# Kernel tuning notes

Measured on AMD Instinct MI355X. Metric: run time of the kernel, lower is better.

Reference implementation:

```python
import jax, jax.numpy as jnp
import numpy as np

B, S, F_ATT, R, A = 1024, 96, 2048, 512, 512  # batch, att_size, att_feat_size, rnn_size, att_hid_size

def setup_inputs() -> dict:
    key = jax.random.key(0)
    ks = jax.random.split(key, 16)
    def lin(k, out_d, in_d):
        s = 1.0 / np.sqrt(in_d)
        kw, kb = jax.random.split(k)
        return (jax.random.uniform(kw, (out_d, in_d), jnp.float32, -s, s),
                jax.random.uniform(kb, (out_d,), jnp.float32, -s, s))
    W_ae, b_ae = lin(ks[0], R, F_ATT)   # att_embed Linear
    W_c,  b_c  = lin(ks[1], A, R)       # ctx2att
    W_s,  b_s  = lin(ks[2], A, R)       # sentinel_embed
    W_h,  b_h  = lin(ks[3], A, R)       # ho_embed
    W_al, b_al = lin(ks[4], 1, A)       # alpha_net
    W_o,  b_o  = lin(ks[5], R, R)       # att2h
    return {
        'h': jax.random.normal(ks[6], (B, R), jnp.float32),
        'sentinel': jax.random.normal(ks[7], (B, R), jnp.float32),
        'att_feats': jax.random.normal(ks[8], (B, S, F_ATT), jnp.float32),
        'W_ae': W_ae, 'b_ae': b_ae, 'W_c': W_c, 'b_c': b_c,
        'W_s': W_s, 'b_s': b_s, 'W_h': W_h, 'b_h': b_h,
        'W_al': W_al, 'b_al': b_al, 'W_o': W_o, 'b_o': b_o,
    }

def reference(h, sentinel, att_feats, W_ae, b_ae, W_c, b_c, W_s, b_s,
              W_h, b_h, W_al, b_al, W_o, b_o):
    # att_embed: Linear(2048->512) + ReLU (dropout = identity in eval)
    att = jax.nn.relu(jnp.einsum('bsf,rf->bsr', att_feats, W_ae) + b_ae)  # [B,S,R]
    att_embd = jnp.einsum('bsr,ar->bsa', att, W_c) + b_c                   # [B,S,A]
    sent_e = sentinel @ W_s.T + b_s                                        # [B,A]
    h_e = h @ W_h.T + b_h                                                  # [B,A]
    # concat sentinel slot in front of attention features
    img_all = jnp.concatenate([sentinel[:, None, :], att], axis=1)         # [B,S+1,R]
    img_all_embed = jnp.concatenate([sent_e[:, None, :], att_embd], axis=1)  # [B,S+1,A]
    hA = jnp.tanh(img_all_embed + h_e[:, None, :])                         # [B,S+1,A]
    logits = jnp.einsum('bsa,a->bs', hA, W_al[0]) + b_al[0]                # [B,S+1]
    alpha = jax.nn.softmax(logits, axis=-1)
    cHat = jnp.einsum('bs,bsr->br', alpha, img_all)                        # [B,R]
    atten_out = cHat + h
    return jnp.tanh(atten_out @ W_o.T + b_o)                               # [B,R]
```

## Files before the change

### kernel.cpp

```cpp
#include <hip/hip_runtime.h>

#define M1 98304
#define RDIM 512
#define FDIM 2048
#define SDIM 96
#define BM 96
#define BK 64

typedef __attribute__((ext_vector_type(8))) __bf16 bf16x8;
typedef __attribute__((ext_vector_type(4))) float f32x4;

__device__ __forceinline__ float bf2f(unsigned short u){
  union { unsigned int i; float f; } v; v.i = ((unsigned int)u) << 16; return v.f;
}
__device__ __forceinline__ unsigned short f2bf(float f){
  union { float f; unsigned int i; } v; v.f = f;
  unsigned int r = v.i + 0x7FFFu + ((v.i >> 16) & 1u);
  return (unsigned short)(r >> 16);
}
__device__ __forceinline__ unsigned short f2bfn(float f){
  __bf16 b = (__bf16)f;
  return __builtin_bit_cast(unsigned short, b);
}
__device__ __forceinline__ float fast_tanh(float x){
  float e = __expf(2.f * x);
  return 1.f - 2.f / (e + 1.f);
}
__device__ __forceinline__ void gld_lds16(const void* g, void* l){
  __builtin_amdgcn_global_load_lds((const __attribute__((address_space(1))) void*)g,
                                   (__attribute__((address_space(3))) void*)l, 16, 0, 0);
}
__device__ __forceinline__ f32x4 mfma16(bf16x8 a, bf16x8 b, f32x4 c){
  return __builtin_amdgcn_mfma_f32_16x16x32_bf16(a, b, c, 0, 0, 0);
}

__device__ __forceinline__ void cat_store_a(const float* __restrict__ src,
                                            unsigned short* __restrict__ dst, int idx){
  float x = src[idx];
  int r = idx >> 9, c = idx & 511;
  unsigned short hi = f2bf(x);
  unsigned short lo = f2bf(x - bf2f(hi));
  unsigned short* p = dst + (long)r * 1536 + c;
  p[0] = hi; p[512] = lo; p[1024] = hi;
}
__device__ __forceinline__ void cat_store_w(const float* __restrict__ src,
                                            unsigned short* __restrict__ dst, int idx){
  float x = src[idx];
  int r = idx >> 9, c = idx & 511;
  unsigned short hi = f2bf(x);
  unsigned short lo = f2bf(x - bf2f(hi));
  unsigned short* p = dst + (long)r * 1536 + c;
  p[0] = hi; p[512] = hi; p[1024] = lo;
}

__global__ void k_convert(const float* W_ae, const float* W_c, const float* W_s,
                          const float* W_h, const float* W_o,
                          const float* h, const float* sent,
                          unsigned short* W_ae_bf, unsigned short* W_c_bf,
                          unsigned short* W_s_cat, unsigned short* W_h_cat,
                          unsigned short* W_o_cat, unsigned short* h_cat,
                          unsigned short* s_cat){
  int idx = blockIdx.x * 256 + threadIdx.x;
  switch (blockIdx.y) {
    case 0: if (idx < 512*2048) W_ae_bf[idx] = f2bf(W_ae[idx]); break;
    case 1: if (idx < 512*512)  W_c_bf[idx]  = f2bf(W_c[idx]);  break;
    case 2: if (idx < 512*512)  cat_store_w(W_s, W_s_cat, idx); break;
    case 3: if (idx < 512*512)  cat_store_w(W_h, W_h_cat, idx); break;
    case 4: if (idx < 512*512)  cat_store_w(W_o, W_o_cat, idx); break;
    case 5: if (idx < 1024*512) cat_store_a(h, h_cat, idx); break;
    case 6: if (idx < 1024*512) cat_store_a(sent, s_cat, idx); break;
  }
}

__global__ __launch_bounds__(512) void k_fused(
    const float* __restrict__ Af, const unsigned short* __restrict__ Wae,
    const float* __restrict__ b_ae,
    const unsigned short* __restrict__ Wcg, const float* __restrict__ b_c,
    const float* __restrict__ h_e, const float* __restrict__ W_al,
    const float* __restrict__ sent_e, const float* __restrict__ sent,
    const float* __restrict__ hvec, unsigned short* __restrict__ atten_cat){
  __shared__ __align__(16) char smem[155648];
  unsigned short* As   = (unsigned short*)smem;
  unsigned short* Bs   = (unsigned short*)(smem + 24576);
  unsigned short* attL = (unsigned short*)smem;
  unsigned short* Wcs  = (unsigned short*)(smem + 98304);
  float* part = (float*)(smem + 131072);
  float* lg   = (float*)(smem + 131072 + 1536);
  float* alp  = (float*)(smem + 131072 + 1536 + 512);
  float* ssum = (float*)(smem + 131072 + 1536 + 1024);

  const int tid = threadIdx.x;
  const int w = tid >> 6, l = tid & 63;
  const int wm = w >> 2, wn = w & 3;
  const int b = blockIdx.x;
  const long m0 = (long)b * BM;
  const int g = l >> 4, r15 = l & 15;
  const int rs = r15 & 7;

  f32x4 acc[3][8];
#pragma unroll
  for (int i = 0; i < 3; ++i)
#pragma unroll
    for (int j = 0; j < 8; ++j) acc[i][j] = f32x4{0.f,0.f,0.f,0.f};

  {
    const int brow_in = l >> 3;
    const int bswz = (l & 7) ^ brow_in;
    const unsigned short* bbase = Wae + (long)(w*64 + brow_in) * FDIM + bswz*8;
    const int NT = FDIM / BK;

    {
#pragma unroll
      for (int q = 0; q < 8; ++q)
        gld_lds16(bbase + (long)q*8*FDIM, Bs + (w*8+q)*512);
      float4 v[3];
#pragma unroll
      for (int s = 0; s < 3; ++s) {
        int c = tid + s*512, row = c >> 4, kq = c & 15;
        v[s] = *reinterpret_cast<const float4*>(Af + (m0+row)*FDIM + kq*4);
      }
#pragma unroll
      for (int s = 0; s < 3; ++s) {
        int c = tid + s*512, row = c >> 4, kq = c & 15;
        ushort4 pk; pk.x=f2bfn(v[s].x); pk.y=f2bfn(v[s].y); pk.z=f2bfn(v[s].z); pk.w=f2bfn(v[s].w);
        *reinterpret_cast<ushort4*>(&As[row*BK + ((kq ^ ((row&7)<<1))<<2)]) = pk;
      }
    }
    __syncthreads();

    int cb = 0;
    for (int kt = 0; kt < NT; ++kt) {
      const int nb = cb ^ 1;
      float4 v[3];
      const bool more = (kt + 1 < NT);
      if (more) {
        const int kof = (kt+1) * BK;
#pragma unroll
        for (int q = 0; q < 8; ++q)
          gld_lds16(bbase + (long)q*8*FDIM + kof, Bs + nb*32768 + (w*8+q)*512);
#pragma unroll
        for (int s = 0; s < 3; ++s) {
          int c = tid + s*512, row = c >> 4, kq = c & 15;
          v[s] = *reinterpret_cast<const float4*>(Af + (m0+row)*FDIM + kof + kq*4);
        }
      }
#pragma unroll
      for (int hh = 0; hh < 2; ++hh) {
        const int ko = ((g + 4*hh) ^ rs) << 3;
        bf16x8 afr[3], bfr[8];
#pragma unroll
        for (int i = 0; i < 3; ++i)
          afr[i] = *reinterpret_cast<const bf16x8*>(&As[cb*6144 + (wm*48 + i*16 + r15)*BK + ko]);
#pragma unroll
        for (int j = 0; j < 8; ++j)
          bfr[j] = *reinterpret_cast<const bf16x8*>(&Bs[cb*32768 + (wn*128 + j*16 + r15)*BK + ko]);
        __builtin_amdgcn_s_setprio(1);
#pragma unroll
        for (int i = 0; i < 3; ++i)
#pragma unroll
          for (int j = 0; j < 8; ++j)
            acc[i][j] = mfma16(afr[i], bfr[j], acc[i][j]);
        __builtin_amdgcn_s_setprio(0);
      }
      if (more) {
#pragma unroll
        for (int s = 0; s < 3; ++s) {
          int c = tid + s*512, row = c >> 4, kq = c & 15;
          ushort4 pk; pk.x=f2bfn(v[s].x); pk.y=f2bfn(v[s].y); pk.z=f2bfn(v[s].z); pk.w=f2bfn(v[s].w);
          *reinterpret_cast<ushort4*>(&As[nb*6144 + row*BK + ((kq ^ ((row&7)<<1))<<2)]) = pk;
        }
        __syncthreads();
        cb = nb;
      }
    }
  }
  __syncthreads();
  {
    float bb[8];
#pragma unroll
    for (int j = 0; j < 8; ++j) bb[j] = b_ae[wn*128 + j*16 + r15];
#pragma unroll
    for (int i = 0; i < 3; ++i)
#pragma unroll
      for (int r = 0; r < 4; ++r) {
        int row = wm*48 + i*16 + g*4 + r;
        int rs8 = row & 7;
#pragma unroll
        for (int j = 0; j < 8; ++j) {
          int col = wn*128 + j*16 + r15;
          float x = acc[i][j][r] + bb[j];
          x = x > 0.f ? x : 0.f;
          attL[row*512 + (((col>>3) ^ rs8)<<3) + (col&7)] = f2bfn(x);
        }
      }
  }
  __syncthreads();

#pragma unroll
  for (int i = 0; i < 3; ++i)
#pragma unroll
    for (int j = 0; j < 8; ++j) acc[i][j] = f32x4{0.f,0.f,0.f,0.f};
  {
    const int crow = l >> 2;
    const int bsl2 = (l & 3) ^ ((l >> 3) & 3);
    const int rs2 = (r15 >> 1) & 3;
    for (int kt = 0; kt < 16; ++kt) {
#pragma unroll
      for (int i = 0; i < 4; ++i)
        gld_lds16(Wcg + (long)(w*64 + i*16 + crow)*RDIM + kt*32 + bsl2*8,
                  Wcs + w*2048 + i*512);
      __syncthreads();
      bf16x8 afr[3], bfr[8];
#pragma unroll
      for (int i = 0; i < 3; ++i) {
        int ra = wm*48 + i*16 + r15;
        int grp = (kt<<2) + g;
        afr[i] = *reinterpret_cast<const bf16x8*>(&attL[ra*512 + ((grp ^ rs)<<3)]);
      }
#pragma unroll
      for (int j = 0; j < 8; ++j)
        bfr[j] = *reinterpret_cast<const bf16x8*>(&Wcs[(wn*128 + j*16 + r15)*32 + ((g ^ rs2)<<3)]);
      __builtin_amdgcn_s_setprio(1);
#pragma unroll
      for (int i = 0; i < 3; ++i)
#pragma unroll
        for (int j = 0; j < 8; ++j)
          acc[i][j] = mfma16(afr[i], bfr[j], acc[i][j]);
      __builtin_amdgcn_s_setprio(0);
      __syncthreads();
    }
  }
  {
    const float* hrow = h_e + (long)b * RDIM;
    float bb2[8], wa[8], he[8];
#pragma unroll
    for (int j = 0; j < 8; ++j) {
      int n = wn*128 + j*16 + r15;
      bb2[j] = b_c[n]; wa[j] = W_al[n]; he[j] = hrow[n];
    }
#pragma unroll
    for (int i = 0; i < 3; ++i)
#pragma unroll
      for (int r = 0; r < 4; ++r) {
        int lrow = wm*48 + i*16 + g*4 + r;
        float s = 0.f;
#pragma unroll
        for (int j = 0; j < 8; ++j) {
          float x = acc[i][j][r] + bb2[j] + he[j];
          s += fast_tanh(x) * wa[j];
        }
        s += __shfl_xor(s, 1); s += __shfl_xor(s, 2);
        s += __shfl_xor(s, 4); s += __shfl_xor(s, 8);
        if (r15 == 0) part[lrow*4 + wn] = s;
      }
  }
  __syncthreads();
  if (tid < 96)
    lg[1+tid] = part[tid*4+0] + part[tid*4+1] + part[tid*4+2] + part[tid*4+3];
  if (tid < 64) {
    float s = 0.f;
    for (int a = tid; a < 512; a += 64)
      s += fast_tanh(sent_e[(long)b*512 + a] + h_e[(long)b*512 + a]) * W_al[a];
    s += __shfl_xor(s, 1); s += __shfl_xor(s, 2); s += __shfl_xor(s, 4);
    s += __shfl_xor(s, 8); s += __shfl_xor(s, 16); s += __shfl_xor(s, 32);
    if (tid == 0) lg[0] = s;
  }
  __syncthreads();
  if (tid < 64) {
    float m = -1e30f;
    for (int i = tid; i < 97; i += 64) m = fmaxf(m, lg[i]);
#pragma unroll
    for (int k = 1; k < 64; k <<= 1) m = fmaxf(m, __shfl_xor(m, k));
    float ss = 0.f;
    for (int i = tid; i < 97; i += 64) { float e = __expf(lg[i] - m); alp[i] = e; ss += e; }
#pragma unroll
    for (int k = 1; k < 64; k <<= 1) ss += __shfl_xor(ss, k);
    if (tid == 0) ssum[0] = ss;
  }
  __syncthreads();
  if (tid < 97) alp[tid] *= (1.f / ssum[0]);
  __syncthreads();
  {
    const int col = tid;
    const int cg = col >> 3, ch = col & 7;
    float accv = alp[0] * sent[(long)b*512 + col];
#pragma unroll 4
    for (int s = 0; s < SDIM; ++s)
      accv += alp[s+1] * bf2f(attL[s*512 + ((cg ^ (s&7))<<3) + ch]);
    float x = accv + hvec[(long)b*512 + col];
    unsigned short hi = f2bf(x);
    unsigned short lo = f2bf(x - bf2f(hi));
    unsigned short* pp = atten_cat + (long)b*1536 + col;
    pp[0] = hi; pp[512] = lo; pp[1024] = hi;
  }
}

__device__ __forceinline__ void small_gemm_body(
    const unsigned short* __restrict__ Abf, const unsigned short* __restrict__ Wb,
    const float* __restrict__ bias, float* __restrict__ Cout, int do_tanh, int bx,
    unsigned short* As, unsigned short* Bs){
  const int tid = threadIdx.x;
  const int w = tid >> 6, l = tid & 63;
  const int wm = w >> 1, wn = w & 1;
  const int m0 = (bx >> 3) * 64, n0 = (bx & 7) * 64;
  const int K = 1536;
  f32x4 acc[2][2];
#pragma unroll
  for (int i = 0; i < 2; ++i)
#pragma unroll
    for (int j = 0; j < 2; ++j) acc[i][j] = f32x4{0.f,0.f,0.f,0.f};

  const int crow = l >> 2;
  const int bsl = (l & 3) ^ ((l >> 3) & 3);

  for (int kt = 0; kt < 48; ++kt) {
    const int k0 = kt * 32;
    gld_lds16(Abf + (long)(m0 + w*16 + crow)*K + k0 + bsl*8, As + w*512);
    gld_lds16(Wb  + (long)(n0 + w*16 + crow)*K + k0 + bsl*8, Bs + w*512);
    __syncthreads();
    bf16x8 afr[2], bfr[2];
    const int g = l >> 4, r15 = l & 15;
    const int rs2 = (r15 >> 1) & 3;
#pragma unroll
    for (int i = 0; i < 2; ++i)
      afr[i] = *reinterpret_cast<const bf16x8*>(As + (wm*32 + i*16 + r15)*32 + ((g ^ rs2)*8));
#pragma unroll
    for (int j = 0; j < 2; ++j)
      bfr[j] = *reinterpret_cast<const bf16x8*>(Bs + (wn*32 + j*16 + r15)*32 + ((g ^ rs2)*8));
#pragma unroll
    for (int i = 0; i < 2; ++i)
#pragma unroll
      for (int j = 0; j < 2; ++j)
        acc[i][j] = mfma16(afr[i], bfr[j], acc[i][j]);
    __syncthreads();
  }
  const int r15 = l & 15, g = l >> 4;
#pragma unroll
  for (int i = 0; i < 2; ++i)
#pragma unroll
    for (int r = 0; r < 4; ++r) {
      int m = m0 + wm*32 + i*16 + g*4 + r;
#pragma unroll
      for (int j = 0; j < 2; ++j) {
        int n = n0 + wn*32 + j*16 + r15;
        float x = acc[i][j][r] + bias[n];
        if (do_tanh) x = fast_tanh(x);
        Cout[(long)m * 512 + n] = x;
      }
    }
}

__global__ __launch_bounds__(256) void k_gemm_small(
    const unsigned short* __restrict__ Abf, const unsigned short* __restrict__ Wb,
    const float* __restrict__ bias, float* __restrict__ Cout, int do_tanh){
  __shared__ __align__(16) unsigned short As[64*32];
  __shared__ __align__(16) unsigned short Bs[64*32];
  small_gemm_body(Abf, Wb, bias, Cout, do_tanh, blockIdx.x, As, Bs);
}

__global__ __launch_bounds__(256) void k_embed2(
    const unsigned short* __restrict__ h_cat, const unsigned short* __restrict__ W_h_cat,
    const float* __restrict__ b_h, float* __restrict__ h_e,
    const unsigned short* __restrict__ s_cat, const unsigned short* __restrict__ W_s_cat,
    const float* __restrict__ b_s, float* __restrict__ sent_e){
  __shared__ __align__(16) unsigned short As[64*32];
  __shared__ __align__(16) unsigned short Bs[64*32];
  if (blockIdx.y == 0) small_gemm_body(h_cat, W_h_cat, b_h, h_e, 0, blockIdx.x, As, Bs);
  else                 small_gemm_body(s_cat, W_s_cat, b_s, sent_e, 0, blockIdx.x, As, Bs);
}

extern "C" void kernel_launch(void* const* d_in, const int* in_sizes, int n_in,
                              void* d_out, int out_size, void* d_ws, size_t ws_size,
                              hipStream_t stream){
  (void)in_sizes; (void)n_in; (void)out_size; (void)ws_size;
  const float* h    = (const float*)d_in[0];
  const float* sent = (const float*)d_in[1];
  const float* feats= (const float*)d_in[2];
  const float* W_ae = (const float*)d_in[3];
  const float* b_ae = (const float*)d_in[4];
  const float* W_c  = (const float*)d_in[5];
  const float* b_c  = (const float*)d_in[6];
  const float* W_s  = (const float*)d_in[7];
  const float* b_s  = (const float*)d_in[8];
  const float* W_h  = (const float*)d_in[9];
  const float* b_h  = (const float*)d_in[10];
  const float* W_al = (const float*)d_in[11];
  const float* W_o  = (const float*)d_in[13];
  const float* b_o  = (const float*)d_in[14];
  float* out = (float*)d_out;

  char* p = (char*)d_ws;
  unsigned short* W_ae_bf = (unsigned short*)p; p += (size_t)512*2048*2;
  unsigned short* W_c_bf  = (unsigned short*)p; p += (size_t)512*512*2;
  unsigned short* W_s_cat = (unsigned short*)p; p += (size_t)512*1536*2;
  unsigned short* W_h_cat = (unsigned short*)p; p += (size_t)512*1536*2;
  unsigned short* W_o_cat = (unsigned short*)p; p += (size_t)512*1536*2;
  unsigned short* h_cat   = (unsigned short*)p; p += (size_t)1024*1536*2;
  unsigned short* s_cat   = (unsigned short*)p; p += (size_t)1024*1536*2;
  unsigned short* at_cat  = (unsigned short*)p; p += (size_t)1024*1536*2;
  float* h_e    = (float*)p; p += (size_t)1024*512*4;
  float* sent_e = (float*)p; p += (size_t)1024*512*4;

  k_convert<<<dim3(4096,7), 256, 0, stream>>>(W_ae, W_c, W_s, W_h, W_o, h, sent,
        W_ae_bf, W_c_bf, W_s_cat, W_h_cat, W_o_cat, h_cat, s_cat);
  k_embed2<<<dim3(128,2), 256, 0, stream>>>(h_cat, W_h_cat, b_h, h_e,
                                            s_cat, W_s_cat, b_s, sent_e);
  k_fused<<<1024, 512, 0, stream>>>(feats, W_ae_bf, b_ae, W_c_bf, b_c,
                                    h_e, W_al, sent_e, sent, h, at_cat);
  k_gemm_small<<<128, 256, 0, stream>>>(at_cat, W_o_cat, b_o, out, 1);
}
```

Before: 450.2 us.

## Deepen A-tile prefetch, register-stage W_c loads, double-buffer small GEMMs

```diff
diff --git a/kernel.cpp b/kernel.cpp
--- a/kernel.cpp
+++ b/kernel.cpp
@@ -9,6 +9,13 @@
 
 typedef __attribute__((ext_vector_type(8))) __bf16 bf16x8;
 typedef __attribute__((ext_vector_type(4))) float f32x4;
+
+#define WAITV6 asm volatile("s_waitcnt vmcnt(6)" ::: "memory")
+#define WAITV3 asm volatile("s_waitcnt vmcnt(3)" ::: "memory")
+#define WAITV0 asm volatile("s_waitcnt vmcnt(0)" ::: "memory")
+#define WAITL0 asm volatile("s_waitcnt lgkmcnt(0)" ::: "memory")
+#define SBAR   __builtin_amdgcn_s_barrier()
+#define SCHED0 __builtin_amdgcn_sched_barrier(0)
 
 __device__ __forceinline__ float bf2f(unsigned short u){
   union { unsigned int i; float f; } v; v.i = ((unsigned int)u) << 16; return v.f;
@@ -60,15 +67,16 @@
                           unsigned short* W_s_cat, unsigned short* W_h_cat,
                           unsigned short* W_o_cat, unsigned short* h_cat,
                           unsigned short* s_cat){
-  int idx = blockIdx.x * 256 + threadIdx.x;
+  const int stride = 1024 * 256;
+  int i0 = blockIdx.x * 256 + threadIdx.x;
   switch (blockIdx.y) {
-    case 0: if (idx < 512*2048) W_ae_bf[idx] = f2bf(W_ae[idx]); break;
-    case 1: if (idx < 512*512)  W_c_bf[idx]  = f2bf(W_c[idx]);  break;
-    case 2: if (idx < 512*512)  cat_store_w(W_s, W_s_cat, idx); break;
-    case 3: if (idx < 512*512)  cat_store_w(W_h, W_h_cat, idx); break;
-    case 4: if (idx < 512*512)  cat_store_w(W_o, W_o_cat, idx); break;
-    case 5: if (idx < 1024*512) cat_store_a(h, h_cat, idx); break;
-    case 6: if (idx < 1024*512) cat_store_a(sent, s_cat, idx); break;
+    case 0: for (int i = i0; i < 512*2048; i += stride) W_ae_bf[i] = f2bf(W_ae[i]); break;
+    case 1: for (int i = i0; i < 512*512;  i += stride) W_c_bf[i]  = f2bf(W_c[i]);  break;
+    case 2: for (int i = i0; i < 512*512;  i += stride) cat_store_w(W_s, W_s_cat, i); break;
+    case 3: for (int i = i0; i < 512*512;  i += stride) cat_store_w(W_h, W_h_cat, i); break;
+    case 4: for (int i = i0; i < 512*512;  i += stride) cat_store_w(W_o, W_o_cat, i); break;
+    case 5: for (int i = i0; i < 1024*512; i += stride) cat_store_a(h, h_cat, i); break;
+    case 6: for (int i = i0; i < 1024*512; i += stride) cat_store_a(sent, s_cat, i); break;
   }
 }
 
@@ -107,43 +115,61 @@
     const int brow_in = l >> 3;
     const int bswz = (l & 7) ^ brow_in;
     const unsigned short* bbase = Wae + (long)(w*64 + brow_in) * FDIM + bswz*8;
+    int arow[3], akq[3], aswz[3];
+    const float* abase[3];
+#pragma unroll
+    for (int s = 0; s < 3; ++s) {
+      int c = tid + s*512;
+      arow[s] = c >> 4; akq[s] = c & 15;
+      abase[s] = Af + (m0 + arow[s])*FDIM + akq[s]*4;
+      aswz[s] = arow[s]*BK + ((akq[s] ^ ((arow[s]&7)<<1))<<2);
+    }
     const int NT = FDIM / BK;
+    float4 d0,d1,d2, e0,e1,e2;
+    float4 f0 = {0,0,0,0}, f1 = {0,0,0,0}, f2 = {0,0,0,0};
 
     {
+      float4 c0 = *reinterpret_cast<const float4*>(abase[0]);
+      float4 c1 = *reinterpret_cast<const float4*>(abase[1]);
+      float4 c2 = *reinterpret_cast<const float4*>(abase[2]);
+      SCHED0;
 #pragma unroll
       for (int q = 0; q < 8; ++q)
         gld_lds16(bbase + (long)q*8*FDIM, Bs + (w*8+q)*512);
-      float4 v[3];
-#pragma unroll
-      for (int s = 0; s < 3; ++s) {
-        int c = tid + s*512, row = c >> 4, kq = c & 15;
-        v[s] = *reinterpret_cast<const float4*>(Af + (m0+row)*FDIM + kq*4);
-      }
-#pragma unroll
-      for (int s = 0; s < 3; ++s) {
-        int c = tid + s*512, row = c >> 4, kq = c & 15;
-        ushort4 pk; pk.x=f2bfn(v[s].x); pk.y=f2bfn(v[s].y); pk.z=f2bfn(v[s].z); pk.w=f2bfn(v[s].w);
-        *reinterpret_cast<ushort4*>(&As[row*BK + ((kq ^ ((row&7)<<1))<<2)]) = pk;
-      }
-    }
-    __syncthreads();
+      SCHED0;
+      d0 = *reinterpret_cast<const float4*>(abase[0] + BK);
+      d1 = *reinterpret_cast<const float4*>(abase[1] + BK);
+      d2 = *reinterpret_cast<const float4*>(abase[2] + BK);
+      e0 = *reinterpret_cast<const float4*>(abase[0] + 2*BK);
+      e1 = *reinterpret_cast<const float4*>(abase[1] + 2*BK);
+      e2 = *reinterpret_cast<const float4*>(abase[2] + 2*BK);
+      SCHED0;
+      ushort4 p0; p0.x=f2bfn(c0.x); p0.y=f2bfn(c0.y); p0.z=f2bfn(c0.z); p0.w=f2bfn(c0.w);
+      ushort4 p1; p1.x=f2bfn(c1.x); p1.y=f2bfn(c1.y); p1.z=f2bfn(c1.z); p1.w=f2bfn(c1.w);
+      ushort4 p2; p2.x=f2bfn(c2.x); p2.y=f2bfn(c2.y); p2.z=f2bfn(c2.z); p2.w=f2bfn(c2.w);
+      *reinterpret_cast<ushort4*>(&As[aswz[0]]) = p0;
+      *reinterpret_cast<ushort4*>(&As[aswz[1]]) = p1;
+      *reinterpret_cast<ushort4*>(&As[aswz[2]]) = p2;
+      WAITV6; WAITL0; SCHED0; SBAR; SCHED0;
+    }
 
     int cb = 0;
     for (int kt = 0; kt < NT; ++kt) {
       const int nb = cb ^ 1;
-      float4 v[3];
-      const bool more = (kt + 1 < NT);
-      if (more) {
+      if (kt + 1 < NT) {
         const int kof = (kt+1) * BK;
 #pragma unroll
         for (int q = 0; q < 8; ++q)
           gld_lds16(bbase + (long)q*8*FDIM + kof, Bs + nb*32768 + (w*8+q)*512);
-#pragma unroll
-        for (int s = 0; s < 3; ++s) {
-          int c = tid + s*512, row = c >> 4, kq = c & 15;
-          v[s] = *reinterpret_cast<const float4*>(Af + (m0+row)*FDIM + kof + kq*4);
-        }
-      }
+      }
+      SCHED0;
+      if (kt + 3 < NT) {
+        const int kof = (kt+3) * BK;
+        f0 = *reinterpret_cast<const float4*>(abase[0] + kof);
+        f1 = *reinterpret_cast<const float4*>(abase[1] + kof);
+        f2 = *reinterpret_cast<const float4*>(abase[2] + kof);
+      }
+      SCHED0;
 #pragma unroll
       for (int hh = 0; hh < 2; ++hh) {
         const int ko = ((g + 4*hh) ^ rs) << 3;
@@ -162,14 +188,16 @@
             acc[i][j] = mfma16(afr[i], bfr[j], acc[i][j]);
         __builtin_amdgcn_s_setprio(0);
       }
-      if (more) {
-#pragma unroll
-        for (int s = 0; s < 3; ++s) {
-          int c = tid + s*512, row = c >> 4, kq = c & 15;
-          ushort4 pk; pk.x=f2bfn(v[s].x); pk.y=f2bfn(v[s].y); pk.z=f2bfn(v[s].z); pk.w=f2bfn(v[s].w);
-          *reinterpret_cast<ushort4*>(&As[nb*6144 + row*BK + ((kq ^ ((row&7)<<1))<<2)]) = pk;
-        }
-        __syncthreads();
+      if (kt + 1 < NT) {
+        ushort4 p0; p0.x=f2bfn(d0.x); p0.y=f2bfn(d0.y); p0.z=f2bfn(d0.z); p0.w=f2bfn(d0.w);
+        ushort4 p1; p1.x=f2bfn(d1.x); p1.y=f2bfn(d1.y); p1.z=f2bfn(d1.z); p1.w=f2bfn(d1.w);
+        ushort4 p2; p2.x=f2bfn(d2.x); p2.y=f2bfn(d2.y); p2.z=f2bfn(d2.z); p2.w=f2bfn(d2.w);
+        *reinterpret_cast<ushort4*>(&As[nb*6144 + aswz[0]]) = p0;
+        *reinterpret_cast<ushort4*>(&As[nb*6144 + aswz[1]]) = p1;
+        *reinterpret_cast<ushort4*>(&As[nb*6144 + aswz[2]]) = p2;
+        d0=e0; d1=e1; d2=e2; e0=f0; e1=f1; e2=f2;
+        if (kt + 3 < NT) { WAITV3; } else { WAITV0; }
+        WAITL0; SCHED0; SBAR; SCHED0;
         cb = nb;
       }
     }
@@ -204,12 +232,24 @@
     const int crow = l >> 2;
     const int bsl2 = (l & 3) ^ ((l >> 3) & 3);
     const int rs2 = (r15 >> 1) & 3;
+    uint4 rr0, rr1, rr2, rr3;
+    rr0 = *reinterpret_cast<const uint4*>(Wcg + (long)(w*64 + 0*16 + crow)*RDIM + bsl2*8);
+    rr1 = *reinterpret_cast<const uint4*>(Wcg + (long)(w*64 + 1*16 + crow)*RDIM + bsl2*8);
+    rr2 = *reinterpret_cast<const uint4*>(Wcg + (long)(w*64 + 2*16 + crow)*RDIM + bsl2*8);
+    rr3 = *reinterpret_cast<const uint4*>(Wcg + (long)(w*64 + 3*16 + crow)*RDIM + bsl2*8);
     for (int kt = 0; kt < 16; ++kt) {
-#pragma unroll
-      for (int i = 0; i < 4; ++i)
-        gld_lds16(Wcg + (long)(w*64 + i*16 + crow)*RDIM + kt*32 + bsl2*8,
-                  Wcs + w*2048 + i*512);
-      __syncthreads();
+      *reinterpret_cast<uint4*>(&Wcs[w*2048 + 0*512 + l*8]) = rr0;
+      *reinterpret_cast<uint4*>(&Wcs[w*2048 + 1*512 + l*8]) = rr1;
+      *reinterpret_cast<uint4*>(&Wcs[w*2048 + 2*512 + l*8]) = rr2;
+      *reinterpret_cast<uint4*>(&Wcs[w*2048 + 3*512 + l*8]) = rr3;
+      if (kt < 15) {
+        const int k0 = (kt+1)*32;
+        rr0 = *reinterpret_cast<const uint4*>(Wcg + (long)(w*64 + 0*16 + crow)*RDIM + k0 + bsl2*8);
+        rr1 = *reinterpret_cast<const uint4*>(Wcg + (long)(w*64 + 1*16 + crow)*RDIM + k0 + bsl2*8);
+        rr2 = *reinterpret_cast<const uint4*>(Wcg + (long)(w*64 + 2*16 + crow)*RDIM + k0 + bsl2*8);
+        rr3 = *reinterpret_cast<const uint4*>(Wcg + (long)(w*64 + 3*16 + crow)*RDIM + k0 + bsl2*8);
+      }
+      WAITL0; SCHED0; SBAR; SCHED0;
       bf16x8 afr[3], bfr[8];
 #pragma unroll
       for (int i = 0; i < 3; ++i) {
@@ -227,7 +267,7 @@
         for (int j = 0; j < 8; ++j)
           acc[i][j] = mfma16(afr[i], bfr[j], acc[i][j]);
       __builtin_amdgcn_s_setprio(0);
-      __syncthreads();
+      WAITL0; SCHED0; SBAR; SCHED0;
     }
   }
   {
@@ -312,27 +352,35 @@
 
   const int crow = l >> 2;
   const int bsl = (l & 3) ^ ((l >> 3) & 3);
-
+  const unsigned short* arow_p = Abf + (long)(m0 + w*16 + crow)*K + bsl*8;
+  const unsigned short* brow_p = Wb  + (long)(n0 + w*16 + crow)*K + bsl*8;
+
+  gld_lds16(arow_p, As + w*512);
+  gld_lds16(brow_p, Bs + w*512);
+  __syncthreads();
+  int cb = 0;
   for (int kt = 0; kt < 48; ++kt) {
-    const int k0 = kt * 32;
-    gld_lds16(Abf + (long)(m0 + w*16 + crow)*K + k0 + bsl*8, As + w*512);
-    gld_lds16(Wb  + (long)(n0 + w*16 + crow)*K + k0 + bsl*8, Bs + w*512);
-    __syncthreads();
+    const int nb = cb ^ 1;
+    if (kt + 1 < 48) {
+      const int k0 = (kt+1) * 32;
+      gld_lds16(arow_p + k0, As + nb*2048 + w*512);
+      gld_lds16(brow_p + k0, Bs + nb*2048 + w*512);
+    }
     bf16x8 afr[2], bfr[2];
     const int g = l >> 4, r15 = l & 15;
     const int rs2 = (r15 >> 1) & 3;
 #pragma unroll
     for (int i = 0; i < 2; ++i)
-      afr[i] = *reinterpret_cast<const bf16x8*>(As + (wm*32 + i*16 + r15)*32 + ((g ^ rs2)*8));
+      afr[i] = *reinterpret_cast<const bf16x8*>(As + cb*2048 + (wm*32 + i*16 + r15)*32 + ((g ^ rs2)*8));
 #pragma unroll
     for (int j = 0; j < 2; ++j)
-      bfr[j] = *reinterpret_cast<const bf16x8*>(Bs + (wn*32 + j*16 + r15)*32 + ((g ^ rs2)*8));
+      bfr[j] = *reinterpret_cast<const bf16x8*>(Bs + cb*2048 + (wn*32 + j*16 + r15)*32 + ((g ^ rs2)*8));
 #pragma unroll
     for (int i = 0; i < 2; ++i)
 #pragma unroll
       for (int j = 0; j < 2; ++j)
         acc[i][j] = mfma16(afr[i], bfr[j], acc[i][j]);
-    __syncthreads();
+    if (kt + 1 < 48) { __syncthreads(); cb = nb; }
   }
   const int r15 = l & 15, g = l >> 4;
 #pragma unroll
@@ -353,8 +401,8 @@
 __global__ __launch_bounds__(256) void k_gemm_small(
     const unsigned short* __restrict__ Abf, const unsigned short* __restrict__ Wb,
     const float* __restrict__ bias, float* __restrict__ Cout, int do_tanh){
-  __shared__ __align__(16) unsigned short As[64*32];
-  __shared__ __align__(16) unsigned short Bs[64*32];
+  __shared__ __align__(16) unsigned short As[2*64*32];
+  __shared__ __align__(16) unsigned short Bs[2*64*32];
   small_gemm_body(Abf, Wb, bias, Cout, do_tanh, blockIdx.x, As, Bs);
 }
 
@@ -363,8 +411,8 @@
     const float* __restrict__ b_h, float* __restrict__ h_e,
     const unsigned short* __restrict__ s_cat, const unsigned short* __restrict__ W_s_cat,
     const float* __restrict__ b_s, float* __restrict__ sent_e){
-  __shared__ __align__(16) unsigned short As[64*32];
-  __shared__ __align__(16) unsigned short Bs[64*32];
+  __shared__ __align__(16) unsigned short As[2*64*32];
+  __shared__ __align__(16) unsigned short Bs[2*64*32];
   if (blockIdx.y == 0) small_gemm_body(h_cat, W_h_cat, b_h, h_e, 0, blockIdx.x, As, Bs);
   else                 small_gemm_body(s_cat, W_s_cat, b_s, sent_e, 0, blockIdx.x, As, Bs);
 }
@@ -401,7 +449,7 @@
   float* h_e    = (float*)p; p += (size_t)1024*512*4;
   float* sent_e = (float*)p; p += (size_t)1024*512*4;
 
-  k_convert<<<dim3(4096,7), 256, 0, stream>>>(W_ae, W_c, W_s, W_h, W_o, h, sent,
+  k_convert<<<dim3(1024,7), 256, 0, stream>>>(W_ae, W_c, W_s, W_h, W_o, h, sent,
         W_ae_bf, W_c_bf, W_s_cat, W_h_cat, W_o_cat, h_cat, s_cat);
   k_embed2<<<dim3(128,2), 256, 0, stream>>>(h_cat, W_h_cat, b_h, h_e,
                                             s_cat, W_s_cat, b_s, sent_e);
```

After: 416.5 us. -7.5%, faster.
